# Kernel optimization log

Measured on AMD Instinct MI355X. Metric: run time of the kernel, lower is better.

The kernel has to match this reference:

```python
import jax, jax.numpy as jnp
import numpy as np

B, H, W, C = 1, 180, 360, 192
WS, SHIFT, NH = 6, 3, 6
MLAT, MLON = H // WS, W // WS
NW = MLAT * MLON
N = WS * WS
HD = C // NH
SCALE = HD ** -0.5
EPS = 1e-5


def _rel_index():
    # earth-specific relative position index: (MLAT, N, N) int32
    ch = np.arange(WS)
    cw = np.arange(WS)
    coords = np.stack(np.meshgrid(ch, cw, indexing='ij')).reshape(2, -1)  # (2, N)
    rel = coords[:, :, None] - coords[:, None, :]                         # (2, N, N)
    idx = (rel[0] + WS - 1) * (2 * WS - 1) + (rel[1] + WS - 1)            # (N, N)
    off = np.arange(MLAT) * (2 * WS - 1) * (2 * WS - 1)                   # per-latitude offset
    return (idx[None, :, :] + off[:, None, None]).astype(np.int32)


def _attn_mask():
    # standard shifted-window mask: (NW, N, N), 0 or -100
    img = np.zeros((H, W), dtype=np.int32)
    cnt = 0
    for hs in (slice(0, -WS), slice(-WS, -SHIFT), slice(-SHIFT, None)):
        for ws_ in (slice(0, -WS), slice(-WS, -SHIFT), slice(-SHIFT, None)):
            img[hs, ws_] = cnt
            cnt += 1
    wins = img.reshape(MLAT, WS, MLON, WS).transpose(0, 2, 1, 3).reshape(NW, N)
    diff = wins[:, None, :] - wins[:, :, None]
    return np.where(diff != 0, -100.0, 0.0).astype(np.float32)

_RPI = jnp.asarray(_rel_index())     # (MLAT, N, N)
_MASK = jnp.asarray(_attn_mask())    # (NW, N, N)


def _layernorm(x, g, b):
    mu = jnp.mean(x, axis=-1, keepdims=True)
    var = jnp.mean(jnp.square(x - mu), axis=-1, keepdims=True)
    return (x - mu) * jax.lax.rsqrt(var + EPS) * g + b


def _window_partition(x):
    # (B, H, W, C) -> (B*NW, N, C)
    x = x.reshape(B, MLAT, WS, MLON, WS, C).transpose(0, 1, 3, 2, 4, 5)
    return x.reshape(B * NW, N, C)


def _window_reverse(w):
    # (B*NW, N, C) -> (B, H, W, C)
    x = w.reshape(B, MLAT, MLON, WS, WS, C).transpose(0, 1, 3, 2, 4, 5)
    return x.reshape(B, H, W, C)


def setup_inputs() -> dict:
    key = jax.random.key(0)
    ks = jax.random.split(key, 6)
    s = 0.02
    return {
        'x': jax.random.normal(ks[0], (B, H * W, C), jnp.float32),
        'norm1_w': jnp.ones((C,), jnp.float32),
        'norm1_b': jnp.zeros((C,), jnp.float32),
        'qkv_w': jax.random.normal(ks[1], (C, 3 * C), jnp.float32) * s,
        'qkv_b': jnp.zeros((3 * C,), jnp.float32),
        'proj_w': jax.random.normal(ks[2], (C, C), jnp.float32) * s,
        'proj_b': jnp.zeros((C,), jnp.float32),
        'bias_table': jax.random.normal(ks[3], (MLAT * (2 * WS - 1) ** 2, NH), jnp.float32) * s,
        'norm2_w': jnp.ones((C,), jnp.float32),
        'norm2_b': jnp.zeros((C,), jnp.float32),
        'fc1_w': jax.random.normal(ks[4], (C, 4 * C), jnp.float32) * s,
        'fc1_b': jnp.zeros((4 * C,), jnp.float32),
        'fc2_w': jax.random.normal(ks[5], (4 * C, C), jnp.float32) * s,
        'fc2_b': jnp.zeros((C,), jnp.float32),
    }


def reference(x, norm1_w, norm1_b, qkv_w, qkv_b, proj_w, proj_b, bias_table,
              norm2_w, norm2_b, fc1_w, fc1_b, fc2_w, fc2_b):
    shortcut = x
    h = _layernorm(x, norm1_w, norm1_b).reshape(B, H, W, C)
    # cyclic shift
    h = jnp.roll(h, shift=(-SHIFT, -SHIFT), axis=(1, 2))
    xw = _window_partition(h)                                   # (B*NW, N, C)

    qkv = xw @ qkv_w + qkv_b                                    # (B_, N, 3C)
    qkv = qkv.reshape(B * NW, N, 3, NH, HD).transpose(2, 0, 3, 1, 4)
    q, k, v = qkv[0], qkv[1], qkv[2]                            # (B_, NH, N, HD)

    # earth-specific relative position bias, gathered per latitude row
    bias = jnp.take(bias_table, _RPI, axis=0)                   # (MLAT, N, N, NH)
    bias = bias.transpose(0, 3, 1, 2)[:, None]                  # (MLAT, 1, NH, N, N)
    bias = jnp.broadcast_to(bias, (MLAT, MLON, NH, N, N)).reshape(NW, NH, N, N)
    bias = bias + _MASK[:, None]                                # add shift mask

    attn = jnp.einsum('bhnd,bhmd->bhnm', q, k) * SCALE + bias
    attn = jax.nn.softmax(attn, axis=-1)
    av = jnp.einsum('bhnm,bhmd->bhnd', attn, v)                 # (B_, NH, N, HD)
    av = av.transpose(0, 2, 1, 3).reshape(B * NW, N, C)
    av = av @ proj_w + proj_b

    h = _window_reverse(av)
    h = jnp.roll(h, shift=(SHIFT, SHIFT), axis=(1, 2)).reshape(B, H * W, C)
    x = shortcut + h

    m = _layernorm(x, norm2_w, norm2_b)
    m = jax.nn.gelu(m @ fc1_w + fc1_b, approximate=False) @ fc2_w + fc2_b
    return x + m
```

## Files before the change

### kernel.cpp

```cpp
#include <hip/hip_runtime.h>
#include <hip/hip_bf16.h>

constexpr int HH   = 180;
constexpr int WW   = 360;
constexpr int CC   = 192;
constexpr int WS   = 6;
constexpr int SHIFT= 3;
constexpr int NH   = 6;
constexpr int MLAT = HH / WS;
constexpr int MLON = WW / WS;
constexpr int NWIN = MLAT * MLON;
constexpr int NTOK = WS * WS;
constexpr int HD   = CC / NH;
constexpr long M_TOK = (long)NWIN * NTOK;
constexpr long M_PAD = 65024;
constexpr float SCALE_F = 0.17677669529663687f;

typedef unsigned short ushort_t;
using bf16x8 = __attribute__((ext_vector_type(8))) short;
using f32x4  = __attribute__((ext_vector_type(4))) float;

static __device__ inline float b2f(ushort_t u) {
    union { float f; unsigned int i; } v; v.i = ((unsigned int)u) << 16; return v.f;
}
static __device__ inline ushort_t f2b(float f) {
    __hip_bfloat16 h = __float2bfloat16(f);
    return *(ushort_t*)&h;
}

static __device__ inline void gload_lds16(const ushort_t* g, ushort_t* l) {
    __builtin_amdgcn_global_load_lds(
        (const __attribute__((address_space(1))) unsigned int*)g,
        (__attribute__((address_space(3))) unsigned int*)l, 16, 0, 0);
}

__global__ void transpose_f2b(const float* __restrict__ in, ushort_t* __restrict__ out,
                              int K, int N) {
    int e = blockIdx.x * 256 + threadIdx.x;
    if (e >= K * N) return;
    int n = e / K, k = e - n * K;
    out[e] = f2b(in[(long)k * N + n]);
}

__global__ void zero_bf16(ushort_t* __restrict__ p, int count) {
    int e = blockIdx.x * 256 + threadIdx.x;
    if (e < count) p[e] = 0;
}

static __device__ inline int region1d(int p, int L) {
    return (p < L - WS) ? 0 : ((p < L - SHIFT) ? 1 : 2);
}

__global__ void bias_mask_precompute(const float* __restrict__ bt, float* __restrict__ bm) {
    int idx = blockIdx.x * 256 + threadIdx.x;
    if (idx >= MLAT * 2 * NH * NTOK * NTOK) return;
    int e = idx;
    int ij = e % (NTOK * NTOK); e /= (NTOK * NTOK);
    int h = e % NH; e /= NH;
    int lt = e % 2;
    int mlat = e / 2;
    int i = ij / NTOK, j = ij - (ij / NTOK) * NTOK;
    int ih = i / WS, iw = i - ih * WS;
    int jh = j / WS, jw = j - jh * WS;
    int bidx = mlat * 121 + (ih - jh + 5) * 11 + (iw - jw + 5);
    float v = bt[bidx * NH + h];
    int mlon = lt ? (MLON - 1) : 0;
    int ri = region1d(mlat * WS + ih, HH) * 3 + region1d(mlon * WS + iw, WW);
    int rj = region1d(mlat * WS + jh, HH) * 3 + region1d(mlon * WS + jw, WW);
    if (ri != rj) v += -100.0f;
    bm[idx] = v;
}

__global__ __launch_bounds__(256) void ln1_window_kernel(
    const float* __restrict__ x, const float* __restrict__ g, const float* __restrict__ b,
    ushort_t* __restrict__ xw)
{
    long t = (long)blockIdx.x * 4 + (threadIdx.x >> 6);
    int lane = threadIdx.x & 63;
    if (t >= M_PAD) return;
    if (t >= M_TOK) {
        ushort_t* o = xw + t * CC;
        o[lane] = 0; o[lane + 64] = 0; o[lane + 128] = 0;
        return;
    }
    int ti = (int)t;
    int w = ti / NTOK, n = ti - w * NTOK;
    int mlat = w / MLON, mlon = w - mlat * MLON;
    int sh = mlat * WS + n / WS, sw = mlon * WS + (n % WS);
    int hh = sh + SHIFT; if (hh >= HH) hh -= HH;
    int ww = sw + SHIFT; if (ww >= WW) ww -= WW;
    const float* row = x + ((long)hh * WW + ww) * CC;
    float v0 = row[lane], v1 = row[lane + 64], v2 = row[lane + 128];
    float s = v0 + v1 + v2;
    float ss = v0 * v0 + v1 * v1 + v2 * v2;
    #pragma unroll
    for (int o = 32; o > 0; o >>= 1) { s += __shfl_xor(s, o, 64); ss += __shfl_xor(ss, o, 64); }
    float mu = s * (1.0f / CC);
    float var = ss * (1.0f / CC) - mu * mu;
    float rinv = rsqrtf(var + 1e-5f);
    ushort_t* o = xw + t * CC;
    o[lane]       = f2b((v0 - mu) * rinv * g[lane]       + b[lane]);
    o[lane + 64]  = f2b((v1 - mu) * rinv * g[lane + 64]  + b[lane + 64]);
    o[lane + 128] = f2b((v2 - mu) * rinv * g[lane + 128] + b[lane + 128]);
}

__global__ __launch_bounds__(256) void ln2_kernel(
    const float* __restrict__ xin, const float* __restrict__ g, const float* __restrict__ b,
    ushort_t* __restrict__ h2)
{
    long t = (long)blockIdx.x * 4 + (threadIdx.x >> 6);
    int lane = threadIdx.x & 63;
    if (t >= M_PAD) return;
    if (t >= M_TOK) {
        ushort_t* o = h2 + t * CC;
        o[lane] = 0; o[lane + 64] = 0; o[lane + 128] = 0;
        return;
    }
    const float* row = xin + t * CC;
    float v0 = row[lane], v1 = row[lane + 64], v2 = row[lane + 128];
    float s = v0 + v1 + v2;
    float ss = v0 * v0 + v1 * v1 + v2 * v2;
    #pragma unroll
    for (int o = 32; o > 0; o >>= 1) { s += __shfl_xor(s, o, 64); ss += __shfl_xor(ss, o, 64); }
    float mu = s * (1.0f / CC);
    float var = ss * (1.0f / CC) - mu * mu;
    float rinv = rsqrtf(var + 1e-5f);
    ushort_t* o = h2 + t * CC;
    o[lane]       = f2b((v0 - mu) * rinv * g[lane]       + b[lane]);
    o[lane + 64]  = f2b((v1 - mu) * rinv * g[lane + 64]  + b[lane + 64]);
    o[lane + 128] = f2b((v2 - mu) * rinv * g[lane + 128] + b[lane + 128]);
}

#define BM 128
#define BN 192
#define BK 32

template<int MODE, int KK>
__global__ __launch_bounds__(512, 3) void gemm_bf16(
    const ushort_t* __restrict__ A, const ushort_t* __restrict__ Bt,
    const float* __restrict__ bias,
    ushort_t* __restrict__ outb, float* __restrict__ outf,
    const float* __restrict__ resid,
    int N, long Mguard, int ncol, int nwg)
{
    constexpr int nk = KK / BK;
    __shared__ __align__(16) ushort_t lds[20480];
    __shared__ int row_map[BM];

    int tid = threadIdx.x;
    int lane = tid & 63;
    int wid = tid >> 6;
    int lr = lane & 15, lg = lane >> 4;
    int wm = wid >> 2, wn = wid & 3;

    int orig = blockIdx.x;
    int q = nwg >> 3, r8 = nwg & 7;
    int xcd = orig & 7, pos = orig >> 3;
    int wg = (xcd < r8 ? xcd * (q + 1) : r8 * (q + 1) + (xcd - r8) * q) + pos;
    int brow = wg / ncol, bcol = wg - brow * ncol;
    long bm0 = (long)brow * BM;
    int n0 = bcol * BN;

    if (MODE == 2 && tid < BM) {
        long t = bm0 + tid;
        if (t < M_TOK) {
            int ti = (int)t;
            int w = ti / NTOK, n = ti - w * NTOK;
            int mlat = w / MLON, mlon = w - mlat * MLON;
            int sh = mlat * WS + n / WS, sw = mlon * WS + (n % WS);
            int hh = sh + SHIFT; if (hh >= HH) hh -= HH;
            int wv = sw + SHIFT; if (wv >= WW) wv -= WW;
            row_map[tid] = hh * WW + wv;
        } else row_map[tid] = -1;
    }

    int a_pos  = tid * 16;
    int a_row  = a_pos >> 6, a_cb = a_pos & 63;
    int a_scol = (a_cb ^ ((a_row & 3) << 4)) >> 1;
    int b_row  = a_row, b_scol = a_scol;
    int b2_pos = 8192 + a_pos;
    int b2_row = b2_pos >> 6, b2_cb = b2_pos & 63;
    int b2_scol = (b2_cb ^ ((b2_row & 3) << 4)) >> 1;

#define STAGE(b, k0) do { \
    char* base = (char*)lds + (b) * 20480; \
    gload_lds16(&A[(bm0 + a_row) * KK + (k0) + a_scol], (ushort_t*)(base + a_pos)); \
    gload_lds16(&Bt[(long)(n0 + b_row) * KK + (k0) + b_scol], (ushort_t*)(base + 8192 + a_pos)); \
    if (tid < 256) \
        gload_lds16(&Bt[(long)(n0 + b2_row) * KK + (k0) + b2_scol], (ushort_t*)(base + 8192 + b2_pos)); \
} while (0)

    f32x4 acc[4][3] = {};

    STAGE(0, 0);
    __syncthreads();

    int xr = (lr & 3) << 4;

    #pragma unroll
    for (int kt = 0; kt < nk; ++kt) {
        if (kt + 1 < nk) STAGE((kt + 1) & 1, (kt + 1) * BK);
        const char* base = (const char*)lds + (kt & 1) * 20480;
        bf16x8 af[4], bfr[3];
        #pragma unroll
        for (int fm = 0; fm < 4; ++fm) {
            int row = wm * 64 + fm * 16 + lr;
            af[fm] = *(const bf16x8*)(base + row * 64 + ((lg * 16) ^ xr));
        }
        #pragma unroll
        for (int fn = 0; fn < 3; ++fn) {
            int row = wn * 48 + fn * 16 + lr;
            bfr[fn] = *(const bf16x8*)(base + 8192 + row * 64 + ((lg * 16) ^ xr));
        }
        #pragma unroll
        for (int fm = 0; fm < 4; ++fm)
            #pragma unroll
            for (int fn = 0; fn < 3; ++fn)
                acc[fm][fn] = __builtin_amdgcn_mfma_f32_16x16x32_bf16(af[fm], bfr[fn], acc[fm][fn], 0, 0, 0);
        __syncthreads();
    }
#undef STAGE

    float bv[3];
    #pragma unroll
    for (int fn = 0; fn < 3; ++fn) bv[fn] = bias[n0 + wn * 48 + fn * 16 + lr];

    if (MODE == 0 || MODE == 1) {
        ushort_t* bb = lds + wid * 768;
        #pragma unroll
        for (int fm = 0; fm < 4; ++fm) {
            #pragma unroll
            for (int fn = 0; fn < 3; ++fn) {
                #pragma unroll
                for (int r = 0; r < 4; ++r) {
                    float v = acc[fm][fn][r] + bv[fn];
                    if (MODE == 1) {
                        float e2 = exp2f(v * -2.4556617f);
                        v = v * __builtin_amdgcn_rcpf(1.0f + e2);
                    }
                    bb[(lg * 4 + r) * 48 + fn * 16 + lr] = f2b(v);
                }
            }
            #pragma unroll
            for (int i = 0; i < 2; ++i) {
                int cid = i * 64 + lane;
                if (cid < 96) {
                    int row = cid / 6, c6 = cid - row * 6;
                    uint4 val = *(const uint4*)&bb[row * 48 + c6 * 8];
                    long grow = bm0 + wm * 64 + fm * 16 + row;
                    *(uint4*)&outb[grow * (long)N + n0 + wn * 48 + c6 * 8] = val;
                }
            }
        }
    } else {
        float* fb = (float*)lds + wid * 768;
        #pragma unroll
        for (int fm = 0; fm < 4; ++fm) {
            #pragma unroll
            for (int fn = 0; fn < 3; ++fn)
                #pragma unroll
                for (int r = 0; r < 4; ++r)
                    fb[(lg * 4 + r) * 48 + fn * 16 + lr] = acc[fm][fn][r] + bv[fn];
            #pragma unroll
            for (int i = 0; i < 3; ++i) {
                int cid = i * 64 + lane;
                int row = cid / 12, c4 = cid - row * 12;
                f32x4 val = *(const f32x4*)&fb[row * 48 + c4 * 4];
                int lrow = wm * 64 + fm * 16 + row;
                int col = wn * 48 + c4 * 4;
                if (MODE == 3) {
                    long grow = bm0 + lrow;
                    if (grow < Mguard) {
                        float* p = &outf[grow * 192 + col];
                        f32x4 old = *(const f32x4*)p;
                        *(f32x4*)p = old + val;
                    }
                } else {
                    int pp = row_map[lrow];
                    if (pp >= 0) {
                        const float* rp = &resid[(long)pp * 192 + col];
                        f32x4 rv = *(const f32x4*)rp;
                        *(f32x4*)&outf[(long)pp * 192 + col] = rv + val;
                    }
                }
            }
        }
    }
}

__global__ __launch_bounds__(256) void attn_mfma_kernel(
    const ushort_t* __restrict__ qkv,
    const float* __restrict__ bm,
    ushort_t* __restrict__ av)
{
    __shared__ __align__(16) ushort_t Pls[4][48][72];
    __shared__ __align__(16) ushort_t Vt[4][32][72];

    int wid = threadIdx.x >> 6, lane = threadIdx.x & 63;
    int unit = blockIdx.x * 4 + wid;
    int w = unit / NH, h = unit - (unit / NH) * NH;
    int mlat = w / MLON, mlon = w - mlat * MLON;
    int lr = lane & 15, lg = lane >> 4;

    const ushort_t* Qb = qkv + (long)w * NTOK * 576 + h * HD;
    const ushort_t* Kb = Qb + 192;
    const ushort_t* Vb = Qb + 384;

    bf16x8 zero8 = {0,0,0,0,0,0,0,0};

    bf16x8 qf[3], kf[3];
    #pragma unroll
    for (int t = 0; t < 3; ++t) {
        int row = t * 16 + lr;
        qf[t] = (row < NTOK) ? *(const bf16x8*)&Qb[(long)row * 576 + 8 * lg] : zero8;
        kf[t] = (row < NTOK) ? *(const bf16x8*)&Kb[(long)row * 576 + 8 * lg] : zero8;
    }
    f32x4 s[3][3] = {};
    #pragma unroll
    for (int mt = 0; mt < 3; ++mt)
        #pragma unroll
        for (int nt = 0; nt < 3; ++nt)
            s[mt][nt] = __builtin_amdgcn_mfma_f32_16x16x32_bf16(qf[mt], kf[nt], s[mt][nt], 0, 0, 0);

    const float* bb = bm + (((mlat * 2 + (mlon == MLON - 1)) * NH) + h) * (NTOK * NTOK);
    bool jv[3];
    #pragma unroll
    for (int nt = 0; nt < 3; ++nt) jv[nt] = (nt * 16 + lr) < NTOK;

    #pragma unroll
    for (int mt = 0; mt < 3; ++mt) {
        #pragma unroll
        for (int r = 0; r < 4; ++r) {
            int i = mt * 16 + lg * 4 + r;
            float v[3];
            #pragma unroll
            for (int nt = 0; nt < 3; ++nt) {
                int j = nt * 16 + lr;
                float t = s[mt][nt][r] * SCALE_F;
                if (i < NTOK && j < NTOK) t += bb[i * NTOK + j];
                v[nt] = t;
            }
            float mx = -1e30f;
            #pragma unroll
            for (int nt = 0; nt < 3; ++nt) if (jv[nt]) mx = fmaxf(mx, v[nt]);
            #pragma unroll
            for (int o = 1; o < 16; o <<= 1) mx = fmaxf(mx, __shfl_xor(mx, o, 64));
            float e[3], sum = 0.f;
            #pragma unroll
            for (int nt = 0; nt < 3; ++nt) { e[nt] = jv[nt] ? __expf(v[nt] - mx) : 0.f; sum += e[nt]; }
            #pragma unroll
            for (int o = 1; o < 16; o <<= 1) sum += __shfl_xor(sum, o, 64);
            float rs = 1.0f / sum;
            #pragma unroll
            for (int nt = 0; nt < 3; ++nt) s[mt][nt][r] = e[nt] * rs;
        }
    }

    #pragma unroll
    for (int mt = 0; mt < 3; ++mt)
        #pragma unroll
        for (int nt = 0; nt < 3; ++nt)
            #pragma unroll
            for (int r = 0; r < 4; ++r)
                Pls[wid][mt * 16 + lg * 4 + r][nt * 16 + lr] = f2b(s[mt][nt][r]);
    #pragma unroll
    for (int it = 0; it < 2; ++it) {
        int idx = it * 64 + lane;
        if (idx < 96) {
            int row = idx >> 1, hf = idx & 1;
            *(uint4*)&Pls[wid][row][48 + hf * 8] = uint4{0, 0, 0, 0};
        }
    }

    #pragma unroll
    for (int it = 0; it < 8; ++it) {
        int idx = it * 64 + lane;
        int row = idx >> 4, c = idx & 15;
        *(unsigned int*)&Vt[wid][row][36 + c * 2] = 0u;
    }
    #pragma unroll
    for (int it = 0; it < 9; ++it) {
        int e = it * 64 + lane;
        int tok = e >> 4, dp = e & 15;
        unsigned int v2 = *(const unsigned int*)&Vb[(long)tok * 576 + dp * 2];
        Vt[wid][dp * 2][tok]     = (ushort_t)(v2 & 0xffffu);
        Vt[wid][dp * 2 + 1][tok] = (ushort_t)(v2 >> 16);
    }

    f32x4 o[3][2] = {};
    #pragma unroll
    for (int kt = 0; kt < 2; ++kt) {
        bf16x8 pa[3], vb[2];
        #pragma unroll
        for (int mt = 0; mt < 3; ++mt)
            pa[mt] = *(const bf16x8*)&Pls[wid][mt * 16 + lr][kt * 32 + 8 * lg];
        #pragma unroll
        for (int nd = 0; nd < 2; ++nd)
            vb[nd] = *(const bf16x8*)&Vt[wid][nd * 16 + lr][kt * 32 + 8 * lg];
        #pragma unroll
        for (int mt = 0; mt < 3; ++mt)
            #pragma unroll
            for (int nd = 0; nd < 2; ++nd)
                o[mt][nd] = __builtin_amdgcn_mfma_f32_16x16x32_bf16(pa[mt], vb[nd], o[mt][nd], 0, 0, 0);
    }

    #pragma unroll
    for (int mt = 0; mt < 3; ++mt)
        #pragma unroll
        for (int nd = 0; nd < 2; ++nd)
            #pragma unroll
            for (int r = 0; r < 4; ++r) {
                int i = mt * 16 + lg * 4 + r;
                if (i < NTOK)
                    av[((long)w * NTOK + i) * CC + h * HD + nd * 16 + lr] = f2b(o[mt][nd][r]);
            }
}

extern "C" void kernel_launch(void* const* d_in, const int* in_sizes, int n_in,
                              void* d_out, int out_size, void* d_ws, size_t ws_size,
                              hipStream_t stream) {
    const float* x        = (const float*)d_in[0];
    const float* n1w      = (const float*)d_in[1];
    const float* n1b      = (const float*)d_in[2];
    const float* qkv_w    = (const float*)d_in[3];
    const float* qkv_b    = (const float*)d_in[4];
    const float* proj_w   = (const float*)d_in[5];
    const float* proj_b   = (const float*)d_in[6];
    const float* btab     = (const float*)d_in[7];
    const float* n2w      = (const float*)d_in[8];
    const float* n2b      = (const float*)d_in[9];
    const float* fc1_w    = (const float*)d_in[10];
    const float* fc1_b    = (const float*)d_in[11];
    const float* fc2_w    = (const float*)d_in[12];
    const float* fc2_b    = (const float*)d_in[13];
    float* out = (float*)d_out;

    char* p = (char*)d_ws;
    ushort_t* xw  = (ushort_t*)p;  p += M_PAD * 192 * 2;
    ushort_t* big = (ushort_t*)p;  p += M_PAD * 768 * 2;
    ushort_t* av  = (ushort_t*)p;  p += M_PAD * 192 * 2;
    ushort_t* wqkv = (ushort_t*)p; p += 576 * 192 * 2;
    ushort_t* wproj= (ushort_t*)p; p += 192 * 192 * 2;
    ushort_t* wfc1 = (ushort_t*)p; p += 768 * 192 * 2;
    ushort_t* wfc2 = (ushort_t*)p; p += 192 * 768 * 2;
    float*    bmask= (float*)p;    p += MLAT * 2 * NH * NTOK * NTOK * 4;

    transpose_f2b<<<(576*192 + 255)/256, 256, 0, stream>>>(qkv_w, wqkv, 192, 576);
    transpose_f2b<<<(192*192 + 255)/256, 256, 0, stream>>>(proj_w, wproj, 192, 192);
    transpose_f2b<<<(768*192 + 255)/256, 256, 0, stream>>>(fc1_w, wfc1, 192, 768);
    transpose_f2b<<<(192*768 + 255)/256, 256, 0, stream>>>(fc2_w, wfc2, 768, 192);
    bias_mask_precompute<<<(MLAT*2*NH*NTOK*NTOK + 255)/256, 256, 0, stream>>>(btab, bmask);
    zero_bf16<<<((int)(M_PAD - M_TOK)*192 + 255)/256, 256, 0, stream>>>(av + M_TOK * 192, (int)(M_PAD - M_TOK) * 192);

    ln1_window_kernel<<<M_PAD / 4, 256, 0, stream>>>(x, n1w, n1b, xw);

    gemm_bf16<0, 192><<<508 * 3, 512, 0, stream>>>(
        xw, wqkv, qkv_b, big, nullptr, nullptr, 576, M_PAD, 3, 508 * 3);

    attn_mfma_kernel<<<NWIN * NH / 4, 256, 0, stream>>>(big, bmask, av);

    gemm_bf16<2, 192><<<508, 512, 0, stream>>>(
        av, wproj, proj_b, nullptr, out, x, 192, M_TOK, 1, 508);

    ln2_kernel<<<M_PAD / 4, 256, 0, stream>>>(out, n2w, n2b, xw);

    gemm_bf16<1, 192><<<508 * 4, 512, 0, stream>>>(
        xw, wfc1, fc1_b, big, nullptr, nullptr, 768, M_PAD, 4, 508 * 4);

    gemm_bf16<3, 768><<<508, 512, 0, stream>>>(
        big, wfc2, fc2_b, nullptr, out, nullptr, 192, M_TOK, 1, 508);
}
```

Measured before the change: 216.6 us.

## Keep attention softmax in registers via transposed S=K·Qᵀ and lane shuffles

Rewrites the window attention kernel to compute the transposed score matrix so softmax rows are reduced across only two shuffle steps. Probabilities are packed to bf16 and redistributed via cross-lane shuffles straight into MFMA operands, so the LDS staging of P and V is no longer needed. The Q scaling is folded into the QKV GEMM epilogue, and the bias/mask table is padded to 48 columns with -1e30 so padded keys need no branches. V is read with strided scalar global loads, and the kernel now loads Q/K rows past the 36 valid tokens without bounds checks, relying on the padded buffer.

```diff
diff --git a/kernel.cpp b/kernel.cpp
--- a/kernel.cpp
+++ b/kernel.cpp
@@ -27,6 +27,11 @@
     __hip_bfloat16 h = __float2bfloat16(f);
     return *(ushort_t*)&h;
 }
+static __device__ inline unsigned int cvtpk(float lo, float hi) {
+    unsigned int r;
+    asm("v_cvt_pk_bf16_f32 %0, %1, %2" : "=v"(r) : "v"(lo), "v"(hi));
+    return r;
+}
 
 static __device__ inline void gload_lds16(const ushort_t* g, ushort_t* l) {
     __builtin_amdgcn_global_load_lds(
@@ -53,13 +58,14 @@
 
 __global__ void bias_mask_precompute(const float* __restrict__ bt, float* __restrict__ bm) {
     int idx = blockIdx.x * 256 + threadIdx.x;
-    if (idx >= MLAT * 2 * NH * NTOK * NTOK) return;
+    if (idx >= MLAT * 2 * NH * 36 * 48) return;
     int e = idx;
-    int ij = e % (NTOK * NTOK); e /= (NTOK * NTOK);
+    int j = e % 48; e /= 48;
+    int i = e % 36; e /= 36;
     int h = e % NH; e /= NH;
     int lt = e % 2;
     int mlat = e / 2;
-    int i = ij / NTOK, j = ij - (ij / NTOK) * NTOK;
+    if (j >= 36) { bm[idx] = -1e30f; return; }
     int ih = i / WS, iw = i - ih * WS;
     int jh = j / WS, jw = j - jh * WS;
     int bidx = mlat * 121 + (ih - jh + 5) * 11 + (iw - jw + 5);
@@ -234,6 +240,9 @@
                 #pragma unroll
                 for (int r = 0; r < 4; ++r) {
                     float v = acc[fm][fn][r] + bv[fn];
+                    if (MODE == 0) {
+                        if (n0 == 0) v *= SCALE_F;
+                    }
                     if (MODE == 1) {
                         float e2 = exp2f(v * -2.4556617f);
                         v = v * __builtin_amdgcn_rcpf(1.0f + e2);
@@ -293,9 +302,6 @@
     const float* __restrict__ bm,
     ushort_t* __restrict__ av)
 {
-    __shared__ __align__(16) ushort_t Pls[4][48][72];
-    __shared__ __align__(16) ushort_t Vt[4][32][72];
-
     int wid = threadIdx.x >> 6, lane = threadIdx.x & 63;
     int unit = blockIdx.x * 4 + wid;
     int w = unit / NH, h = unit - (unit / NH) * NH;
@@ -306,114 +312,108 @@
     const ushort_t* Kb = Qb + 192;
     const ushort_t* Vb = Qb + 384;
 
-    bf16x8 zero8 = {0,0,0,0,0,0,0,0};
-
-    bf16x8 qf[3], kf[3];
+    bf16x8 kf[3], qf[3];
     #pragma unroll
     for (int t = 0; t < 3; ++t) {
-        int row = t * 16 + lr;
-        qf[t] = (row < NTOK) ? *(const bf16x8*)&Qb[(long)row * 576 + 8 * lg] : zero8;
-        kf[t] = (row < NTOK) ? *(const bf16x8*)&Kb[(long)row * 576 + 8 * lg] : zero8;
-    }
-    f32x4 s[3][3] = {};
+        kf[t] = *(const bf16x8*)&Kb[(long)(t * 16 + lr) * 576 + 8 * lg];
+        qf[t] = *(const bf16x8*)&Qb[(long)(t * 16 + lr) * 576 + 8 * lg];
+    }
+    f32x4 st[3][3] = {};
     #pragma unroll
     for (int mt = 0; mt < 3; ++mt)
         #pragma unroll
-        for (int nt = 0; nt < 3; ++nt)
-            s[mt][nt] = __builtin_amdgcn_mfma_f32_16x16x32_bf16(qf[mt], kf[nt], s[mt][nt], 0, 0, 0);
-
-    const float* bb = bm + (((mlat * 2 + (mlon == MLON - 1)) * NH) + h) * (NTOK * NTOK);
-    bool jv[3];
-    #pragma unroll
-    for (int nt = 0; nt < 3; ++nt) jv[nt] = (nt * 16 + lr) < NTOK;
-
-    #pragma unroll
-    for (int mt = 0; mt < 3; ++mt) {
-        #pragma unroll
-        for (int r = 0; r < 4; ++r) {
-            int i = mt * 16 + lg * 4 + r;
-            float v[3];
-            #pragma unroll
-            for (int nt = 0; nt < 3; ++nt) {
-                int j = nt * 16 + lr;
-                float t = s[mt][nt][r] * SCALE_F;
-                if (i < NTOK && j < NTOK) t += bb[i * NTOK + j];
-                v[nt] = t;
+        for (int qt = 0; qt < 3; ++qt)
+            st[mt][qt] = __builtin_amdgcn_mfma_f32_16x16x32_bf16(kf[mt], qf[qt], st[mt][qt], 0, 0, 0);
+
+    bf16x8 vf[2][2];
+    #pragma unroll
+    for (int nd = 0; nd < 2; ++nd)
+        #pragma unroll
+        for (int kt = 0; kt < 2; ++kt)
+            #pragma unroll
+            for (int j = 0; j < 8; ++j)
+                ((short*)&vf[nd][kt])[j] =
+                    (short)Vb[(long)(kt * 32 + 8 * lg + j) * 576 + nd * 16 + lr];
+
+    const float* bb = bm + (((mlat * 2 + (mlon == MLON - 1)) * NH) + h) * (36 * 48);
+
+    f32x4 o[2][3] = {};
+    int src0 = ((2 * (lg & 1)) << 4) | lr;
+    int src1 = src0 + 16;
+
+    #pragma unroll
+    for (int qt = 0; qt < 3; ++qt) {
+        int qrow = qt * 16 + lr;
+        int qq = qrow < 36 ? qrow : 35;
+        float v[3][4];
+        #pragma unroll
+        for (int mt = 0; mt < 3; ++mt) {
+            f32x4 b4 = *(const f32x4*)&bb[qq * 48 + mt * 16 + 4 * lg];
+            #pragma unroll
+            for (int r = 0; r < 4; ++r) v[mt][r] = st[mt][qt][r] + b4[r];
+        }
+        float mx = v[0][0];
+        #pragma unroll
+        for (int mt = 0; mt < 3; ++mt)
+            #pragma unroll
+            for (int r = 0; r < 4; ++r) mx = fmaxf(mx, v[mt][r]);
+        mx = fmaxf(mx, __shfl_xor(mx, 16, 64));
+        mx = fmaxf(mx, __shfl_xor(mx, 32, 64));
+        float p[3][4], sum = 0.f;
+        #pragma unroll
+        for (int mt = 0; mt < 3; ++mt)
+            #pragma unroll
+            for (int r = 0; r < 4; ++r) { p[mt][r] = __expf(v[mt][r] - mx); sum += p[mt][r]; }
+        sum += __shfl_xor(sum, 16, 64);
+        sum += __shfl_xor(sum, 32, 64);
+        float rs = 1.0f / sum;
+
+        unsigned int pk[3][2];
+        #pragma unroll
+        for (int mt = 0; mt < 3; ++mt) {
+            pk[mt][0] = cvtpk(p[mt][0] * rs, p[mt][1] * rs);
+            pk[mt][1] = cvtpk(p[mt][2] * rs, p[mt][3] * rs);
+        }
+        unsigned int f0[4], f1[4];
+        {
+            unsigned int a, b;
+            a = (unsigned)__shfl((int)pk[0][0], src0, 64); b = (unsigned)__shfl((int)pk[1][0], src0, 64);
+            f0[0] = (lg < 2) ? a : b;
+            a = (unsigned)__shfl((int)pk[0][1], src0, 64); b = (unsigned)__shfl((int)pk[1][1], src0, 64);
+            f0[1] = (lg < 2) ? a : b;
+            a = (unsigned)__shfl((int)pk[0][0], src1, 64); b = (unsigned)__shfl((int)pk[1][0], src1, 64);
+            f0[2] = (lg < 2) ? a : b;
+            a = (unsigned)__shfl((int)pk[0][1], src1, 64); b = (unsigned)__shfl((int)pk[1][1], src1, 64);
+            f0[3] = (lg < 2) ? a : b;
+            f1[0] = (lg < 2) ? (unsigned)__shfl((int)pk[2][0], src0, 64) : 0u;
+            f1[1] = (lg < 2) ? (unsigned)__shfl((int)pk[2][1], src0, 64) : 0u;
+            f1[2] = (lg < 2) ? (unsigned)__shfl((int)pk[2][0], src1, 64) : 0u;
+            f1[3] = (lg < 2) ? (unsigned)__shfl((int)pk[2][1], src1, 64) : 0u;
+        }
+        union { unsigned int u[4]; bf16x8 v8; } pf0, pf1;
+        pf0.u[0] = f0[0]; pf0.u[1] = f0[1]; pf0.u[2] = f0[2]; pf0.u[3] = f0[3];
+        pf1.u[0] = f1[0]; pf1.u[1] = f1[1]; pf1.u[2] = f1[2]; pf1.u[3] = f1[3];
+
+        #pragma unroll
+        for (int nd = 0; nd < 2; ++nd) {
+            o[nd][qt] = __builtin_amdgcn_mfma_f32_16x16x32_bf16(vf[nd][0], pf0.v8, o[nd][qt], 0, 0, 0);
+            o[nd][qt] = __builtin_amdgcn_mfma_f32_16x16x32_bf16(vf[nd][1], pf1.v8, o[nd][qt], 0, 0, 0);
+        }
+    }
+
+    #pragma unroll
+    for (int qt = 0; qt < 3; ++qt) {
+        int qrow = qt * 16 + lr;
+        if (qrow < NTOK) {
+            #pragma unroll
+            for (int nd = 0; nd < 2; ++nd) {
+                uint2 pkd;
+                pkd.x = cvtpk(o[nd][qt][0], o[nd][qt][1]);
+                pkd.y = cvtpk(o[nd][qt][2], o[nd][qt][3]);
+                *(uint2*)&av[((long)w * NTOK + qrow) * CC + h * HD + nd * 16 + 4 * lg] = pkd;
             }
-            float mx = -1e30f;
-            #pragma unroll
-            for (int nt = 0; nt < 3; ++nt) if (jv[nt]) mx = fmaxf(mx, v[nt]);
-            #pragma unroll
-            for (int o = 1; o < 16; o <<= 1) mx = fmaxf(mx, __shfl_xor(mx, o, 64));
-            float e[3], sum = 0.f;
-            #pragma unroll
-            for (int nt = 0; nt < 3; ++nt) { e[nt] = jv[nt] ? __expf(v[nt] - mx) : 0.f; sum += e[nt]; }
-            #pragma unroll
-            for (int o = 1; o < 16; o <<= 1) sum += __shfl_xor(sum, o, 64);
-            float rs = 1.0f / sum;
-            #pragma unroll
-            for (int nt = 0; nt < 3; ++nt) s[mt][nt][r] = e[nt] * rs;
-        }
-    }
-
-    #pragma unroll
-    for (int mt = 0; mt < 3; ++mt)
-        #pragma unroll
-        for (int nt = 0; nt < 3; ++nt)
-            #pragma unroll
-            for (int r = 0; r < 4; ++r)
-                Pls[wid][mt * 16 + lg * 4 + r][nt * 16 + lr] = f2b(s[mt][nt][r]);
-    #pragma unroll
-    for (int it = 0; it < 2; ++it) {
-        int idx = it * 64 + lane;
-        if (idx < 96) {
-            int row = idx >> 1, hf = idx & 1;
-            *(uint4*)&Pls[wid][row][48 + hf * 8] = uint4{0, 0, 0, 0};
-        }
-    }
-
-    #pragma unroll
-    for (int it = 0; it < 8; ++it) {
-        int idx = it * 64 + lane;
-        int row = idx >> 4, c = idx & 15;
-        *(unsigned int*)&Vt[wid][row][36 + c * 2] = 0u;
-    }
-    #pragma unroll
-    for (int it = 0; it < 9; ++it) {
-        int e = it * 64 + lane;
-        int tok = e >> 4, dp = e & 15;
-        unsigned int v2 = *(const unsigned int*)&Vb[(long)tok * 576 + dp * 2];
-        Vt[wid][dp * 2][tok]     = (ushort_t)(v2 & 0xffffu);
-        Vt[wid][dp * 2 + 1][tok] = (ushort_t)(v2 >> 16);
-    }
-
-    f32x4 o[3][2] = {};
-    #pragma unroll
-    for (int kt = 0; kt < 2; ++kt) {
-        bf16x8 pa[3], vb[2];
-        #pragma unroll
-        for (int mt = 0; mt < 3; ++mt)
-            pa[mt] = *(const bf16x8*)&Pls[wid][mt * 16 + lr][kt * 32 + 8 * lg];
-        #pragma unroll
-        for (int nd = 0; nd < 2; ++nd)
-            vb[nd] = *(const bf16x8*)&Vt[wid][nd * 16 + lr][kt * 32 + 8 * lg];
-        #pragma unroll
-        for (int mt = 0; mt < 3; ++mt)
-            #pragma unroll
-            for (int nd = 0; nd < 2; ++nd)
-                o[mt][nd] = __builtin_amdgcn_mfma_f32_16x16x32_bf16(pa[mt], vb[nd], o[mt][nd], 0, 0, 0);
-    }
-
-    #pragma unroll
-    for (int mt = 0; mt < 3; ++mt)
-        #pragma unroll
-        for (int nd = 0; nd < 2; ++nd)
-            #pragma unroll
-            for (int r = 0; r < 4; ++r) {
-                int i = mt * 16 + lg * 4 + r;
-                if (i < NTOK)
-                    av[((long)w * NTOK + i) * CC + h * HD + nd * 16 + lr] = f2b(o[mt][nd][r]);
-            }
+        }
+    }
 }
 
 extern "C" void kernel_launch(void* const* d_in, const int* in_sizes, int n_in,
@@ -443,13 +443,13 @@
     ushort_t* wproj= (ushort_t*)p; p += 192 * 192 * 2;
     ushort_t* wfc1 = (ushort_t*)p; p += 768 * 192 * 2;
     ushort_t* wfc2 = (ushort_t*)p; p += 192 * 768 * 2;
-    float*    bmask= (float*)p;    p += MLAT * 2 * NH * NTOK * NTOK * 4;
+    float*    bmask= (float*)p;    p += MLAT * 2 * NH * 36 * 48 * 4;
 
     transpose_f2b<<<(576*192 + 255)/256, 256, 0, stream>>>(qkv_w, wqkv, 192, 576);
     transpose_f2b<<<(192*192 + 255)/256, 256, 0, stream>>>(proj_w, wproj, 192, 192);
     transpose_f2b<<<(768*192 + 255)/256, 256, 0, stream>>>(fc1_w, wfc1, 192, 768);
     transpose_f2b<<<(192*768 + 255)/256, 256, 0, stream>>>(fc2_w, wfc2, 768, 192);
-    bias_mask_precompute<<<(MLAT*2*NH*NTOK*NTOK + 255)/256, 256, 0, stream>>>(btab, bmask);
+    bias_mask_precompute<<<(MLAT*2*NH*36*48 + 255)/256, 256, 0, stream>>>(btab, bmask);
     zero_bf16<<<((int)(M_PAD - M_TOK)*192 + 255)/256, 256, 0, stream>>>(av + M_TOK * 192, (int)(M_PAD - M_TOK) * 192);
 
     ln1_window_kernel<<<M_PAD / 4, 256, 0, stream>>>(x, n1w, n1b, xw);
```

New measurement: 201.8 us. 6.8% less time.
